# Kernel tuning notes

Measured on AMD Instinct MI355X. Metric: run time of the kernel, lower is better.

Reference implementation:

```python
import jax, jax.numpy as jnp
import numpy as np

B, N, C = 2, 2048, 1024
H = 16
D = C // H  # head_dim = 64

def setup_inputs() -> dict:
    key = jax.random.key(0)
    ks = jax.random.split(key, 5)
    s = 0.02
    return {
        "x": jax.random.normal(ks[0], (B, N, C), dtype=jnp.float32),
        "qkv_w": jax.random.normal(ks[1], (C, 3 * C), dtype=jnp.float32) * s,
        "qkv_b": jax.random.normal(ks[2], (3 * C,), dtype=jnp.float32) * s,
        "proj_w": jax.random.normal(ks[3], (C, C), dtype=jnp.float32) * s,
        "proj_b": jax.random.normal(ks[4], (C,), dtype=jnp.float32) * s,
    }

def reference(x, qkv_w, qkv_b, proj_w, proj_b):
    b, n, c = x.shape
    scale = (c // H) ** -0.5
    qkv = x @ qkv_w + qkv_b                      # (B, N, 3C)
    qkv = qkv.reshape(b, n, 3, H, D)
    q, k, v = jnp.moveaxis(qkv, 2, 0)            # each (B, N, H, D)
    # scores: (B, H, N, N)
    attn = jnp.einsum('bnhd,bmhd->bhnm', q, k) * scale
    attn = jax.nn.softmax(attn, axis=-1)
    out = jnp.einsum('bhnm,bmhd->bnhd', attn, v).reshape(b, n, c)
    out = out @ proj_w + proj_b
    return out
```

## Files before the change

kernel.cpp:

```cpp
#include <hip/hip_runtime.h>
#include <cstdint>
#include <cstddef>

typedef __bf16 bf16x8 __attribute__((ext_vector_type(8)));
typedef __bf16 bf16x2v __attribute__((ext_vector_type(2)));
typedef unsigned short u16;
typedef u16 u16x8v __attribute__((ext_vector_type(8)));
typedef float  f32x4  __attribute__((ext_vector_type(4)));
typedef unsigned int u32;

#define MFMA16(a, b, c) __builtin_amdgcn_mfma_f32_16x16x32_bf16((a), (b), (c), 0, 0, 0)
#define ASYNC16(g, l)                                                              \
  __builtin_amdgcn_global_load_lds(                                                \
      (const __attribute__((address_space(1))) unsigned int*)(g),                  \
      (__attribute__((address_space(3))) unsigned int*)(l), 16, 0, 0)

__device__ __forceinline__ u16 f2bf(float f) {
  unsigned u = __builtin_bit_cast(unsigned, f);
  u += 0x7fffu + ((u >> 16) & 1u);
  return (u16)(u >> 16);
}

__device__ __forceinline__ u32 cvt2(float a, float b) {
  bf16x2v t;
  t[0] = (__bf16)a;
  t[1] = (__bf16)b;
  return __builtin_bit_cast(u32, t);
}

#define SEQ 2048
#define CH  1024
#define NH  16
#define HD  64
#define QSCALE 0.18033688011112042f

__global__ void __launch_bounds__(256) prep_kernel(const float* __restrict__ x,
                                                   const float* __restrict__ qkv_w,
                                                   const float* __restrict__ proj_w,
                                                   u16* __restrict__ xb,
                                                   u16* __restrict__ wqkvt,
                                                   u16* __restrict__ wprojt) {
  __shared__ u16 t[64][68];
  int bx = blockIdx.x;
  int tx = threadIdx.x;
  if (bx < 4096) {
    int i = bx * 256 + tx;
    float4 v = ((const float4*)x)[i];
    ushort4 o;
    o.x = f2bf(v.x); o.y = f2bf(v.y); o.z = f2bf(v.z); o.w = f2bf(v.w);
    ((ushort4*)xb)[i] = o;
    return;
  }
  const float* in; u16* out; int R, C, c0, r0;
  if (bx < 4096 + 768) {
    int i = bx - 4096;
    in = qkv_w; out = wqkvt; R = 1024; C = 3072;
    c0 = (i % 48) * 64; r0 = (i / 48) * 64;
  } else {
    int i = bx - 4864;
    in = proj_w; out = wprojt; R = 1024; C = 1024;
    c0 = (i % 16) * 64; r0 = (i / 16) * 64;
  }
  int rr = tx >> 6, cc = tx & 63;
#pragma unroll
  for (int i = 0; i < 16; ++i) {
    int r = i * 4 + rr;
    t[r][cc] = f2bf(in[(size_t)(r0 + r) * C + c0 + cc]);
  }
  __syncthreads();
#pragma unroll
  for (int i = 0; i < 16; ++i) {
    int r = i * 4 + rr;
    out[(size_t)(c0 + r) * R + r0 + cc] = t[cc][r];
  }
}

template <int MT>
__global__ void __launch_bounds__(256) gemm_kernel(const u16* __restrict__ A,
                                                   const u16* __restrict__ Bt,
                                                   const float* __restrict__ bias,
                                                   u16* __restrict__ qk,
                                                   u16* __restrict__ vtout,
                                                   float* __restrict__ outf,
                                                   int K, int mode) {
  constexpr int R = MT * 32;
  __shared__ alignas(16) u16 smem[2 * R * 64 + 2 * 128 * 64];
  auto As = (u16(*)[R * 64])smem;
  auto Bs = (u16(*)[128 * 64])(smem + 2 * R * 64);
  int tid = threadIdx.x;
  int lane = tid & 63, wave = tid >> 6;
  int wm = wave >> 1, wn = wave & 1;
  int qr = lane & 15, quad = lane >> 4;
  size_t rowA = (size_t)blockIdx.y * R;
  size_t rowB = (size_t)blockIdx.x * 128;

  int klr = lane >> 3;
  int kcs = (lane & 7) ^ klr;

  f32x4 acc[MT][4];
#pragma unroll
  for (int mt = 0; mt < MT; ++mt)
#pragma unroll
    for (int nt = 0; nt < 4; ++nt) acc[mt][nt] = (f32x4){0.f, 0.f, 0.f, 0.f};

  auto stage = [&](int buf, int k0) {
#pragma unroll
    for (int i = 0; i < R / 32; ++i) {
      int ar = wave * (R / 4) + i * 8;
      ASYNC16(A + (rowA + ar + klr) * K + k0 + kcs * 8, &As[buf][ar * 64 + lane * 8]);
    }
#pragma unroll
    for (int i = 0; i < 4; ++i) {
      int br = wave * 32 + i * 8;
      ASYNC16(Bt + (rowB + br + klr) * K + k0 + kcs * 8, &Bs[buf][br * 64 + lane * 8]);
    }
  };

  stage(0, 0);
  int iters = K >> 6;
  for (int t = 0; t < iters; ++t) {
    int cur = t & 1;
    __syncthreads();
    if (t + 1 < iters) stage(cur ^ 1, (t + 1) * 64);
#pragma unroll
    for (int ks = 0; ks < 2; ++ks) {
      bf16x8 af[MT], bfr[4];
#pragma unroll
      for (int mt = 0; mt < MT; ++mt) {
        int row = wm * (MT * 16) + mt * 16 + qr;
        af[mt] = *(const bf16x8*)&As[cur][row * 64 + (((ks * 4 + quad) ^ (qr & 7)) << 3)];
      }
#pragma unroll
      for (int nt = 0; nt < 4; ++nt) {
        int row = wn * 64 + nt * 16 + qr;
        bfr[nt] = *(const bf16x8*)&Bs[cur][row * 64 + (((ks * 4 + quad) ^ (qr & 7)) << 3)];
      }
#pragma unroll
      for (int mt = 0; mt < MT; ++mt)
#pragma unroll
        for (int nt = 0; nt < 4; ++nt)
          acc[mt][nt] = MFMA16(af[mt], bfr[nt], acc[mt][nt]);
    }
    __syncthreads();
  }

  __syncthreads();

  if (mode == 1) {
    float* epf = (float*)smem;
#pragma unroll
    for (int nt = 0; nt < 4; ++nt) {
      int cl = wn * 64 + nt * 16 + qr;
      float bv = bias[rowB + cl];
#pragma unroll
      for (int mt = 0; mt < MT; ++mt) {
        int rl = wm * (MT * 16) + mt * 16 + quad * 4;
#pragma unroll
        for (int r = 0; r < 4; ++r)
          epf[(rl + r) * 132 + cl] = acc[mt][nt][r] + bv;
      }
    }
    __syncthreads();
    int rr = wave * 2 + (lane >> 5);
    int cc = (lane & 31) * 4;
#pragma unroll
    for (int p = 0; p < R / 8; ++p) {
      int row = p * 8 + rr;
      float4 v = *(const float4*)&epf[row * 132 + cc];
      *(float4*)&outf[(rowA + row) * 1024 + rowB + cc] = v;
    }
  } else if ((int)rowB < 2048) {
    float sc = ((int)rowB < 1024) ? QSCALE : 1.0f;
    u16* ep = smem;
#pragma unroll
    for (int nt = 0; nt < 4; ++nt) {
      int cl = wn * 64 + nt * 16 + qr;
      float bv = bias[rowB + cl];
#pragma unroll
      for (int mt = 0; mt < MT; ++mt) {
        int rl = wm * (MT * 16) + mt * 16 + quad * 4;
#pragma unroll
        for (int r = 0; r < 4; ++r)
          ep[(rl + r) * 136 + cl] = f2bf((acc[mt][nt][r] + bv) * sc);
      }
    }
    __syncthreads();
    int rr = wave * 4 + (lane >> 4);
    int cc = (lane & 15) * 8;
#pragma unroll
    for (int p = 0; p < R / 16; ++p) {
      int row = p * 16 + rr;
      u16x8v v = *(const u16x8v*)&ep[row * 136 + cc];
      *(u16x8v*)&qk[(rowA + row) * 2048 + rowB + cc] = v;
    }
  } else {
    u16* ep = smem;
#pragma unroll
    for (int nt = 0; nt < 4; ++nt) {
      int cl = wn * 64 + nt * 16 + qr;
      float bv = bias[rowB + cl];
#pragma unroll
      for (int mt = 0; mt < MT; ++mt) {
        int rl = wm * (MT * 16) + mt * 16 + quad * 4;
        ushort4 pv;
        pv.x = f2bf(acc[mt][nt][0] + bv);
        pv.y = f2bf(acc[mt][nt][1] + bv);
        pv.z = f2bf(acc[mt][nt][2] + bv);
        pv.w = f2bf(acc[mt][nt][3] + bv);
        *(ushort4*)&ep[cl * 136 + rl] = pv;
      }
    }
    __syncthreads();
    int batch = (int)(rowA >> 11);
    int n_base = (int)(rowA & 2047);
    int rr = wave * 4 + (lane >> 4);
    int cc = (lane & 15) * 8;
#pragma unroll
    for (int p = 0; p < 8; ++p) {
      int d = p * 16 + rr;
      int cglob = (int)rowB - 2048 + d;
      int bh_ = batch * 16 + (cglob >> 6);
      u16x8v v = *(const u16x8v*)&ep[d * 136 + cc];
      *(u16x8v*)&vtout[(size_t)bh_ * 131072 + (size_t)(cglob & 63) * 2048 + n_base + cc] = v;
    }
  }
}

__global__ void __launch_bounds__(256) attn_kernel(const u16* __restrict__ qkbuf,
                                                   const u16* __restrict__ vt,
                                                   u16* __restrict__ out) {
  __shared__ alignas(16) u16 kbuf[2][128 * 64];
  __shared__ alignas(16) u16 vbuf[2][64 * 128];
  __shared__ alignas(16) u16 pbuf[4][32 * 64];
  int bh = blockIdx.x;
  int b = bh >> 4, h = bh & 15;
  int m0 = blockIdx.y * 128;
  int tid = threadIdx.x;
  int lane = tid & 63, wave = tid >> 6;
  int qr = lane & 15, quad = lane >> 4;

  const u16* kbase = qkbuf + (size_t)(b * SEQ) * 2048 + 1024 + h * 64;
  const u16* vtbase = vt + (size_t)bh * 64 * SEQ;
  u16* pw = &pbuf[wave][0];

  int klr = lane >> 3;
  int kcs = (lane & 7) ^ klr;

  const u16* qbase = qkbuf + (size_t)(b * SEQ + m0 + wave * 32) * 2048 + h * 64;
  bf16x8 qf[2][2];
#pragma unroll
  for (int mt = 0; mt < 2; ++mt)
#pragma unroll
    for (int ks = 0; ks < 2; ++ks)
      qf[mt][ks] = *(const bf16x8*)&qbase[(size_t)(mt * 16 + qr) * 2048 + ks * 32 + quad * 8];

  const bf16x8 vone = __builtin_bit_cast(bf16x8, (u16x8v)((u16)0x3F80));

  f32x4 o[2][4], l5[2];
#pragma unroll
  for (int mt = 0; mt < 2; ++mt) {
    l5[mt] = (f32x4){0.f, 0.f, 0.f, 0.f};
#pragma unroll
    for (int dt = 0; dt < 4; ++dt) o[mt][dt] = (f32x4){0.f, 0.f, 0.f, 0.f};
  }

  auto stage = [&](int buf, int n0) {
#pragma unroll
    for (int i = 0; i < 4; ++i) {
      int kr = wave * 32 + i * 8 + klr;
      ASYNC16(kbase + (size_t)(n0 + kr) * 2048 + kcs * 8,
              &kbuf[buf][(wave * 32 + i * 8) * 64 + lane * 8]);
    }
#pragma unroll
    for (int i = 0; i < 4; ++i) {
      int vr = wave * 16 + i * 4 + (lane >> 4);
      int vcs = ((lane & 7) ^ (vr & 7)) | (lane & 8);
      ASYNC16(vtbase + (size_t)vr * 2048 + n0 + vcs * 8,
              &vbuf[buf][(wave * 16 + i * 4) * 128 + lane * 8]);
    }
  };

  stage(0, 0);

  for (int t = 0; t < 16; ++t) {
    int cur = t & 1;
    __syncthreads();

    if (t + 1 < 16) stage(cur ^ 1, (t + 1) * 128);

#pragma unroll
    for (int sp = 0; sp < 2; ++sp) {
      const u16* kb = &kbuf[cur][sp * 64 * 64];
      const u16* vb = &vbuf[cur][0];

      bf16x8 kf[4][2];
#pragma unroll
      for (int nt = 0; nt < 4; ++nt)
#pragma unroll
        for (int ks = 0; ks < 2; ++ks)
          kf[nt][ks] =
              *(const bf16x8*)&kb[(nt * 16 + qr) * 64 + (((ks * 4 + quad) ^ (qr & 7)) << 3)];

#pragma unroll
      for (int mt = 0; mt < 2; ++mt)
#pragma unroll
        for (int nt = 0; nt < 4; ++nt) {
          f32x4 z = (f32x4){0.f, 0.f, 0.f, 0.f};
          z = MFMA16(kf[nt][0], qf[mt][0], z);
          z = MFMA16(kf[nt][1], qf[mt][1], z);
          float p0 = __builtin_amdgcn_exp2f(z[0]);
          float p1 = __builtin_amdgcn_exp2f(z[1]);
          float p2 = __builtin_amdgcn_exp2f(z[2]);
          float p3 = __builtin_amdgcn_exp2f(z[3]);
          uint2 pk;
          pk.x = cvt2(p0, p1);
          pk.y = cvt2(p2, p3);
          int nb = nt * 16 + quad * 4;
          int addr = (mt * 16 + qr) * 64 + ((((nb >> 3) ^ (qr & 7)) << 3) | (nb & 7));
          *(uint2*)&pw[addr] = pk;
        }

      bf16x8 vf[4][2];
#pragma unroll
      for (int dt = 0; dt < 4; ++dt)
#pragma unroll
        for (int ks = 0; ks < 2; ++ks)
          vf[dt][ks] = *(const bf16x8*)&vb[(dt * 16 + qr) * 128 +
                                           ((sp * 8 + ((ks * 4 + quad) ^ (qr & 7))) << 3)];

      bf16x8 pf[2][2];
#pragma unroll
      for (int mt = 0; mt < 2; ++mt)
#pragma unroll
        for (int ks = 0; ks < 2; ++ks)
          pf[mt][ks] =
              *(const bf16x8*)&pw[(mt * 16 + qr) * 64 + (((ks * 4 + quad) ^ (qr & 7)) << 3)];

#pragma unroll
      for (int mt = 0; mt < 2; ++mt) {
#pragma unroll
        for (int dt = 0; dt < 4; ++dt) {
          o[mt][dt] = MFMA16(pf[mt][0], vf[dt][0], o[mt][dt]);
          o[mt][dt] = MFMA16(pf[mt][1], vf[dt][1], o[mt][dt]);
        }
        l5[mt] = MFMA16(pf[mt][0], vone, l5[mt]);
        l5[mt] = MFMA16(pf[mt][1], vone, l5[mt]);
      }
    }
  }

  u16* obase = out + (size_t)(b * SEQ + m0 + wave * 32) * CH + h * 64;
#pragma unroll
  for (int mt = 0; mt < 2; ++mt)
#pragma unroll
    for (int r = 0; r < 4; ++r) {
      float inv = 1.0f / l5[mt][r];
#pragma unroll
      for (int dt = 0; dt < 4; ++dt)
        obase[(size_t)(mt * 16 + quad * 4 + r) * CH + dt * 16 + qr] = f2bf(o[mt][dt][r] * inv);
    }
}

extern "C" void kernel_launch(void* const* d_in, const int* in_sizes, int n_in,
                              void* d_out, int out_size, void* d_ws, size_t ws_size,
                              hipStream_t stream) {
  const float* x      = (const float*)d_in[0];
  const float* qkv_w  = (const float*)d_in[1];
  const float* qkv_b  = (const float*)d_in[2];
  const float* proj_w = (const float*)d_in[3];
  const float* proj_b = (const float*)d_in[4];
  float* out = (float*)d_out;

  char* w = (char*)d_ws;
  u16* qkqk   = (u16*)w;
  u16* xb     = (u16*)(w + 16777216);
  u16* wprojt = (u16*)(w + 25165824);
  u16* wqkvt  = (u16*)(w + 27262976);
  u16* vt     = (u16*)(w + 33554432);
  u16* attn_bf = xb;

  prep_kernel<<<5120, 256, 0, stream>>>(x, qkv_w, proj_w, xb, wqkvt, wprojt);
  gemm_kernel<4><<<dim3(24, 32), 256, 0, stream>>>(xb, wqkvt, qkv_b, qkqk, vt, nullptr, 1024, 0);
  attn_kernel<<<dim3(32, 16), 256, 0, stream>>>(qkqk, vt, attn_bf);
  gemm_kernel<2><<<dim3(8, 64), 256, 0, stream>>>(attn_bf, wprojt, proj_b, nullptr, nullptr, out, 1024, 1);
}
```

Measured before the change: 179.9 us.

## Load K and V tiles directly from global memory instead of LDS staging

```diff
diff --git a/kernel.cpp b/kernel.cpp
--- a/kernel.cpp
+++ b/kernel.cpp
@@ -229,8 +229,6 @@
 __global__ void __launch_bounds__(256) attn_kernel(const u16* __restrict__ qkbuf,
                                                    const u16* __restrict__ vt,
                                                    u16* __restrict__ out) {
-  __shared__ alignas(16) u16 kbuf[2][128 * 64];
-  __shared__ alignas(16) u16 vbuf[2][64 * 128];
   __shared__ alignas(16) u16 pbuf[4][32 * 64];
   int bh = blockIdx.x;
   int b = bh >> 4, h = bh & 15;
@@ -243,9 +241,6 @@
   const u16* vtbase = vt + (size_t)bh * 64 * SEQ;
   u16* pw = &pbuf[wave][0];
 
-  int klr = lane >> 3;
-  int kcs = (lane & 7) ^ klr;
-
   const u16* qbase = qkbuf + (size_t)(b * SEQ + m0 + wave * 32) * 2048 + h * 64;
   bf16x8 qf[2][2];
 #pragma unroll
@@ -264,88 +259,61 @@
     for (int dt = 0; dt < 4; ++dt) o[mt][dt] = (f32x4){0.f, 0.f, 0.f, 0.f};
   }
 
-  auto stage = [&](int buf, int n0) {
-#pragma unroll
-    for (int i = 0; i < 4; ++i) {
-      int kr = wave * 32 + i * 8 + klr;
-      ASYNC16(kbase + (size_t)(n0 + kr) * 2048 + kcs * 8,
-              &kbuf[buf][(wave * 32 + i * 8) * 64 + lane * 8]);
-    }
-#pragma unroll
-    for (int i = 0; i < 4; ++i) {
-      int vr = wave * 16 + i * 4 + (lane >> 4);
-      int vcs = ((lane & 7) ^ (vr & 7)) | (lane & 8);
-      ASYNC16(vtbase + (size_t)vr * 2048 + n0 + vcs * 8,
-              &vbuf[buf][(wave * 16 + i * 4) * 128 + lane * 8]);
-    }
-  };
-
-  stage(0, 0);
-
-  for (int t = 0; t < 16; ++t) {
-    int cur = t & 1;
-    __syncthreads();
-
-    if (t + 1 < 16) stage(cur ^ 1, (t + 1) * 128);
-
-#pragma unroll
-    for (int sp = 0; sp < 2; ++sp) {
-      const u16* kb = &kbuf[cur][sp * 64 * 64];
-      const u16* vb = &vbuf[cur][0];
-
-      bf16x8 kf[4][2];
-#pragma unroll
-      for (int nt = 0; nt < 4; ++nt)
-#pragma unroll
-        for (int ks = 0; ks < 2; ++ks)
-          kf[nt][ks] =
-              *(const bf16x8*)&kb[(nt * 16 + qr) * 64 + (((ks * 4 + quad) ^ (qr & 7)) << 3)];
-
-#pragma unroll
-      for (int mt = 0; mt < 2; ++mt)
-#pragma unroll
-        for (int nt = 0; nt < 4; ++nt) {
-          f32x4 z = (f32x4){0.f, 0.f, 0.f, 0.f};
-          z = MFMA16(kf[nt][0], qf[mt][0], z);
-          z = MFMA16(kf[nt][1], qf[mt][1], z);
-          float p0 = __builtin_amdgcn_exp2f(z[0]);
-          float p1 = __builtin_amdgcn_exp2f(z[1]);
-          float p2 = __builtin_amdgcn_exp2f(z[2]);
-          float p3 = __builtin_amdgcn_exp2f(z[3]);
-          uint2 pk;
-          pk.x = cvt2(p0, p1);
-          pk.y = cvt2(p2, p3);
-          int nb = nt * 16 + quad * 4;
-          int addr = (mt * 16 + qr) * 64 + ((((nb >> 3) ^ (qr & 7)) << 3) | (nb & 7));
-          *(uint2*)&pw[addr] = pk;
-        }
-
-      bf16x8 vf[4][2];
-#pragma unroll
-      for (int dt = 0; dt < 4; ++dt)
-#pragma unroll
-        for (int ks = 0; ks < 2; ++ks)
-          vf[dt][ks] = *(const bf16x8*)&vb[(dt * 16 + qr) * 128 +
-                                           ((sp * 8 + ((ks * 4 + quad) ^ (qr & 7))) << 3)];
-
-      bf16x8 pf[2][2];
-#pragma unroll
-      for (int mt = 0; mt < 2; ++mt)
-#pragma unroll
-        for (int ks = 0; ks < 2; ++ks)
-          pf[mt][ks] =
-              *(const bf16x8*)&pw[(mt * 16 + qr) * 64 + (((ks * 4 + quad) ^ (qr & 7)) << 3)];
-
-#pragma unroll
-      for (int mt = 0; mt < 2; ++mt) {
-#pragma unroll
-        for (int dt = 0; dt < 4; ++dt) {
-          o[mt][dt] = MFMA16(pf[mt][0], vf[dt][0], o[mt][dt]);
-          o[mt][dt] = MFMA16(pf[mt][1], vf[dt][1], o[mt][dt]);
-        }
-        l5[mt] = MFMA16(pf[mt][0], vone, l5[mt]);
-        l5[mt] = MFMA16(pf[mt][1], vone, l5[mt]);
-      }
+  for (int t = 0; t < 32; ++t) {
+    const u16* kt = kbase + (size_t)(t * 64) * 2048;
+    const int n0 = t * 64;
+
+    bf16x8 kf[4][2];
+#pragma unroll
+    for (int nt = 0; nt < 4; ++nt)
+#pragma unroll
+      for (int ks = 0; ks < 2; ++ks)
+        kf[nt][ks] = *(const bf16x8*)&kt[(size_t)(nt * 16 + qr) * 2048 + ks * 32 + quad * 8];
+
+    bf16x8 vf[4][2];
+#pragma unroll
+    for (int dt = 0; dt < 4; ++dt)
+#pragma unroll
+      for (int ks = 0; ks < 2; ++ks)
+        vf[dt][ks] =
+            *(const bf16x8*)&vtbase[(size_t)(dt * 16 + qr) * 2048 + n0 + ks * 32 + quad * 8];
+
+#pragma unroll
+    for (int mt = 0; mt < 2; ++mt)
+#pragma unroll
+      for (int nt = 0; nt < 4; ++nt) {
+        f32x4 z = (f32x4){0.f, 0.f, 0.f, 0.f};
+        z = MFMA16(kf[nt][0], qf[mt][0], z);
+        z = MFMA16(kf[nt][1], qf[mt][1], z);
+        float p0 = __builtin_amdgcn_exp2f(z[0]);
+        float p1 = __builtin_amdgcn_exp2f(z[1]);
+        float p2 = __builtin_amdgcn_exp2f(z[2]);
+        float p3 = __builtin_amdgcn_exp2f(z[3]);
+        uint2 pk;
+        pk.x = cvt2(p0, p1);
+        pk.y = cvt2(p2, p3);
+        int nb = nt * 16 + quad * 4;
+        int addr = (mt * 16 + qr) * 64 + ((((nb >> 3) ^ (qr & 7)) << 3) | (nb & 7));
+        *(uint2*)&pw[addr] = pk;
+      }
+
+    bf16x8 pf[2][2];
+#pragma unroll
+    for (int mt = 0; mt < 2; ++mt)
+#pragma unroll
+      for (int ks = 0; ks < 2; ++ks)
+        pf[mt][ks] =
+            *(const bf16x8*)&pw[(mt * 16 + qr) * 64 + (((ks * 4 + quad) ^ (qr & 7)) << 3)];
+
+#pragma unroll
+    for (int mt = 0; mt < 2; ++mt) {
+#pragma unroll
+      for (int dt = 0; dt < 4; ++dt) {
+        o[mt][dt] = MFMA16(pf[mt][0], vf[dt][0], o[mt][dt]);
+        o[mt][dt] = MFMA16(pf[mt][1], vf[dt][1], o[mt][dt]);
+      }
+      l5[mt] = MFMA16(pf[mt][0], vone, l5[mt]);
+      l5[mt] = MFMA16(pf[mt][1], vone, l5[mt]);
     }
   }
 
```

Result: slower. 246.7 us (+37.1%).

## Add 256x256-tile 8-wave GEMM for QKV projection with double-buffered LDS pipeline

Applied to the files above, without the earlier changes.

```diff
diff --git a/kernel.cpp b/kernel.cpp
--- a/kernel.cpp
+++ b/kernel.cpp
@@ -226,6 +226,184 @@
   }
 }
 
+#define G256_LDSA(buf, ks)                                                         \
+  {                                                                                \
+    const u16* base_ = &smem[(buf) * 2 * 8192 + wm * 8192];                        \
+    _Pragma("unroll") for (int mt = 0; mt < 8; ++mt)                               \
+        afr[mt] = *(const bf16x8*)&base_[(mt * 16 + qr) * 64 +                     \
+                                         ((((ks) * 4 + quad) ^ (qr & 7)) << 3)];   \
+  }
+#define G256_LDSB(buf, ks, np)                                                     \
+  {                                                                                \
+    const u16* base_ = &smem[32768 + (buf) * 2 * 8192 + (wn >> 1) * 8192];         \
+    _Pragma("unroll") for (int u = 0; u < 2; ++u)                                  \
+        bfr[u] = *(const bf16x8*)&base_[((wn & 1) * 64 + ((np) * 2 + u) * 16 + qr) * 64 + \
+                                        ((((ks) * 4 + quad) ^ (qr & 7)) << 3)];    \
+  }
+#define G256_MMA(np)                                                               \
+  {                                                                                \
+    __builtin_amdgcn_s_setprio(1);                                                 \
+    _Pragma("unroll") for (int mt = 0; mt < 8; ++mt) {                             \
+      acc[mt][(np) * 2] = MFMA16(afr[mt], bfr[0], acc[mt][(np) * 2]);              \
+      acc[mt][(np) * 2 + 1] = MFMA16(afr[mt], bfr[1], acc[mt][(np) * 2 + 1]);      \
+    }                                                                              \
+    __builtin_amdgcn_s_setprio(0);                                                 \
+  }
+#define G256_STAGE_A(buf, t)                                                       \
+  _Pragma("unroll") for (int h = 0; h < 2; ++h)                                    \
+  _Pragma("unroll") for (int i = 0; i < 2; ++i) {                                  \
+    int rl = i * 64 + wave * 8;                                                    \
+    ASYNC16(A + (rowA + h * 128 + rl + klr) * 1024 + (t) * 64 + kcs * 8,           \
+            &smem[(buf) * 2 * 8192 + h * 8192 + rl * 64 + lane * 8]);              \
+  }
+#define G256_STAGE_B(buf, t)                                                       \
+  _Pragma("unroll") for (int h = 0; h < 2; ++h)                                    \
+  _Pragma("unroll") for (int i = 0; i < 2; ++i) {                                  \
+    int rl = i * 64 + wave * 8;                                                    \
+    ASYNC16(Bt + (rowB + h * 128 + rl + klr) * 1024 + (t) * 64 + kcs * 8,          \
+            &smem[32768 + (buf) * 2 * 8192 + h * 8192 + rl * 64 + lane * 8]);      \
+  }
+#define G256_BAR() __builtin_amdgcn_s_barrier()
+#define G256_VM0() asm volatile("s_waitcnt vmcnt(0)" ::: "memory")
+
+__global__ void __launch_bounds__(512) gemm256_kernel(const u16* __restrict__ A,
+                                                      const u16* __restrict__ Bt,
+                                                      const float* __restrict__ bias,
+                                                      u16* __restrict__ qk,
+                                                      u16* __restrict__ vtout) {
+  __shared__ alignas(16) u16 smem[65536];
+  int tid = threadIdx.x;
+  int lane = tid & 63, wave = tid >> 6;
+  int wm = wave >> 2, wn = wave & 3;
+  int qr = lane & 15, quad = lane >> 4;
+  int klr = lane >> 3;
+  int kcs = (lane & 7) ^ klr;
+
+  size_t rowA = (size_t)blockIdx.y * 256;
+  size_t rowB = (size_t)blockIdx.x * 256;
+
+  f32x4 acc[8][4];
+#pragma unroll
+  for (int mt = 0; mt < 8; ++mt)
+#pragma unroll
+    for (int nt = 0; nt < 4; ++nt) acc[mt][nt] = (f32x4){0.f, 0.f, 0.f, 0.f};
+
+  bf16x8 afr[8], bfr[2];
+
+  G256_STAGE_A(0, 0);
+  G256_STAGE_B(0, 0);
+  G256_VM0();
+
+  for (int j = 0; j < 8; ++j) {
+    G256_BAR();
+    G256_STAGE_A(1, 2 * j + 1);
+    G256_STAGE_B(1, 2 * j + 1);
+    G256_LDSA(0, 0);
+    G256_LDSB(0, 0, 0);
+    G256_MMA(0);
+    G256_BAR();
+    G256_LDSB(0, 0, 1);
+    G256_MMA(1);
+    G256_BAR();
+    G256_LDSA(0, 1);
+    G256_LDSB(0, 1, 0);
+    G256_MMA(0);
+    G256_BAR();
+    G256_LDSB(0, 1, 1);
+    G256_MMA(1);
+    G256_VM0();
+    G256_BAR();
+    if (j + 1 < 8) {
+      G256_STAGE_A(0, 2 * j + 2);
+      G256_STAGE_B(0, 2 * j + 2);
+    }
+    G256_LDSA(1, 0);
+    G256_LDSB(1, 0, 0);
+    G256_MMA(0);
+    G256_BAR();
+    G256_LDSB(1, 0, 1);
+    G256_MMA(1);
+    G256_BAR();
+    G256_LDSA(1, 1);
+    G256_LDSB(1, 1, 0);
+    G256_MMA(0);
+    G256_BAR();
+    G256_LDSB(1, 1, 1);
+    G256_MMA(1);
+    G256_VM0();
+  }
+  __syncthreads();
+
+  int bx = blockIdx.x;
+  float bv[4];
+#pragma unroll
+  for (int nt = 0; nt < 4; ++nt) bv[nt] = bias[rowB + wn * 64 + nt * 16 + qr];
+
+  u16* ep = smem;
+  if (bx < 8) {
+    float sc = (bx < 4) ? QSCALE : 1.0f;
+#pragma unroll
+    for (int cm = 0; cm < 2; ++cm) {
+      if (wm == cm) {
+#pragma unroll
+        for (int mt = 0; mt < 8; ++mt)
+#pragma unroll
+          for (int nt = 0; nt < 4; ++nt) {
+            int rl = mt * 16 + quad * 4;
+            int cl = wn * 64 + nt * 16 + qr;
+#pragma unroll
+            for (int r = 0; r < 4; ++r)
+              ep[(rl + r) * 264 + cl] = f2bf((acc[mt][nt][r] + bv[nt]) * sc);
+          }
+      }
+      __syncthreads();
+      int row = tid >> 5;
+      int c0 = (tid & 31) * 8;
+#pragma unroll
+      for (int p = 0; p < 8; ++p) {
+        int rr = p * 16 + row;
+        u16x8v v = *(const u16x8v*)&ep[rr * 264 + c0];
+        *(u16x8v*)&qk[(rowA + cm * 128 + rr) * 2048 + rowB + c0] = v;
+      }
+      __syncthreads();
+    }
+  } else {
+    int batch = (int)(rowA >> 11);
+    int n_base = (int)(rowA & 2047);
+    int dbase = (int)rowB - 2048;
+#pragma unroll
+    for (int cd = 0; cd < 2; ++cd) {
+      if ((wn >> 1) == cd) {
+#pragma unroll
+        for (int mt = 0; mt < 8; ++mt)
+#pragma unroll
+          for (int nt = 0; nt < 4; ++nt) {
+            int dl = (wn & 1) * 64 + nt * 16 + qr;
+            int nl = wm * 128 + mt * 16 + quad * 4;
+            ushort4 pv;
+            pv.x = f2bf(acc[mt][nt][0] + bv[nt]);
+            pv.y = f2bf(acc[mt][nt][1] + bv[nt]);
+            pv.z = f2bf(acc[mt][nt][2] + bv[nt]);
+            pv.w = f2bf(acc[mt][nt][3] + bv[nt]);
+            *(ushort4*)&ep[dl * 264 + nl] = pv;
+          }
+      }
+      __syncthreads();
+      int dl = tid >> 5;
+      int n0 = (tid & 31) * 8;
+#pragma unroll
+      for (int p = 0; p < 8; ++p) {
+        int dd = p * 16 + dl;
+        int dglob = dbase + cd * 128 + dd;
+        int bh_ = batch * 16 + (dglob >> 6);
+        u16x8v v = *(const u16x8v*)&ep[dd * 264 + n0];
+        *(u16x8v*)&vtout[(size_t)bh_ * 131072 + (size_t)(dglob & 63) * 2048 + n_base + n0] = v;
+      }
+      __syncthreads();
+    }
+  }
+}
+
 __global__ void __launch_bounds__(256) attn_kernel(const u16* __restrict__ qkbuf,
                                                    const u16* __restrict__ vt,
                                                    u16* __restrict__ out) {
@@ -380,7 +558,7 @@
   u16* attn_bf = xb;
 
   prep_kernel<<<5120, 256, 0, stream>>>(x, qkv_w, proj_w, xb, wqkvt, wprojt);
-  gemm_kernel<4><<<dim3(24, 32), 256, 0, stream>>>(xb, wqkvt, qkv_b, qkqk, vt, nullptr, 1024, 0);
+  gemm256_kernel<<<dim3(12, 16), 512, 0, stream>>>(xb, wqkvt, qkv_b, qkqk, vt);
   attn_kernel<<<dim3(32, 16), 256, 0, stream>>>(qkqk, vt, attn_bf);
   gemm_kernel<2><<<dim3(8, 64), 256, 0, stream>>>(attn_bf, wprojt, proj_b, nullptr, nullptr, out, 1024, 1);
 }
```

Result: no change. 182.8 us (+1.6%).

## Split attention work across eight waves with sixteen query rows each

Applied to the files above, without the earlier changes.

```diff
diff --git a/kernel.cpp b/kernel.cpp
--- a/kernel.cpp
+++ b/kernel.cpp
@@ -226,12 +226,12 @@
   }
 }
 
-__global__ void __launch_bounds__(256) attn_kernel(const u16* __restrict__ qkbuf,
-                                                   const u16* __restrict__ vt,
-                                                   u16* __restrict__ out) {
+__global__ void __launch_bounds__(512, 4) attn_kernel(const u16* __restrict__ qkbuf,
+                                                      const u16* __restrict__ vt,
+                                                      u16* __restrict__ out) {
   __shared__ alignas(16) u16 kbuf[2][128 * 64];
   __shared__ alignas(16) u16 vbuf[2][64 * 128];
-  __shared__ alignas(16) u16 pbuf[4][32 * 64];
+  __shared__ alignas(16) u16 pbuf[8][16 * 64];
   int bh = blockIdx.x;
   int b = bh >> 4, h = bh & 15;
   int m0 = blockIdx.y * 128;
@@ -246,37 +246,32 @@
   int klr = lane >> 3;
   int kcs = (lane & 7) ^ klr;
 
-  const u16* qbase = qkbuf + (size_t)(b * SEQ + m0 + wave * 32) * 2048 + h * 64;
-  bf16x8 qf[2][2];
-#pragma unroll
-  for (int mt = 0; mt < 2; ++mt)
-#pragma unroll
-    for (int ks = 0; ks < 2; ++ks)
-      qf[mt][ks] = *(const bf16x8*)&qbase[(size_t)(mt * 16 + qr) * 2048 + ks * 32 + quad * 8];
+  const u16* qbase = qkbuf + (size_t)(b * SEQ + m0 + wave * 16) * 2048 + h * 64;
+  bf16x8 qf[2];
+#pragma unroll
+  for (int ks = 0; ks < 2; ++ks)
+    qf[ks] = *(const bf16x8*)&qbase[(size_t)qr * 2048 + ks * 32 + quad * 8];
 
   const bf16x8 vone = __builtin_bit_cast(bf16x8, (u16x8v)((u16)0x3F80));
 
-  f32x4 o[2][4], l5[2];
-#pragma unroll
-  for (int mt = 0; mt < 2; ++mt) {
-    l5[mt] = (f32x4){0.f, 0.f, 0.f, 0.f};
-#pragma unroll
-    for (int dt = 0; dt < 4; ++dt) o[mt][dt] = (f32x4){0.f, 0.f, 0.f, 0.f};
-  }
+  f32x4 o[4], l5;
+  l5 = (f32x4){0.f, 0.f, 0.f, 0.f};
+#pragma unroll
+  for (int dt = 0; dt < 4; ++dt) o[dt] = (f32x4){0.f, 0.f, 0.f, 0.f};
 
   auto stage = [&](int buf, int n0) {
 #pragma unroll
-    for (int i = 0; i < 4; ++i) {
-      int kr = wave * 32 + i * 8 + klr;
+    for (int i = 0; i < 2; ++i) {
+      int kr = wave * 16 + i * 8 + klr;
       ASYNC16(kbase + (size_t)(n0 + kr) * 2048 + kcs * 8,
-              &kbuf[buf][(wave * 32 + i * 8) * 64 + lane * 8]);
-    }
-#pragma unroll
-    for (int i = 0; i < 4; ++i) {
-      int vr = wave * 16 + i * 4 + (lane >> 4);
+              &kbuf[buf][(wave * 16 + i * 8) * 64 + lane * 8]);
+    }
+#pragma unroll
+    for (int i = 0; i < 2; ++i) {
+      int vr = wave * 8 + i * 4 + (lane >> 4);
       int vcs = ((lane & 7) ^ (vr & 7)) | (lane & 8);
       ASYNC16(vtbase + (size_t)vr * 2048 + n0 + vcs * 8,
-              &vbuf[buf][(wave * 16 + i * 4) * 128 + lane * 8]);
+              &vbuf[buf][(wave * 8 + i * 4) * 128 + lane * 8]);
     }
   };
 
@@ -302,23 +297,21 @@
               *(const bf16x8*)&kb[(nt * 16 + qr) * 64 + (((ks * 4 + quad) ^ (qr & 7)) << 3)];
 
 #pragma unroll
-      for (int mt = 0; mt < 2; ++mt)
-#pragma unroll
-        for (int nt = 0; nt < 4; ++nt) {
-          f32x4 z = (f32x4){0.f, 0.f, 0.f, 0.f};
-          z = MFMA16(kf[nt][0], qf[mt][0], z);
-          z = MFMA16(kf[nt][1], qf[mt][1], z);
-          float p0 = __builtin_amdgcn_exp2f(z[0]);
-          float p1 = __builtin_amdgcn_exp2f(z[1]);
-          float p2 = __builtin_amdgcn_exp2f(z[2]);
-          float p3 = __builtin_amdgcn_exp2f(z[3]);
-          uint2 pk;
-          pk.x = cvt2(p0, p1);
-          pk.y = cvt2(p2, p3);
-          int nb = nt * 16 + quad * 4;
-          int addr = (mt * 16 + qr) * 64 + ((((nb >> 3) ^ (qr & 7)) << 3) | (nb & 7));
-          *(uint2*)&pw[addr] = pk;
-        }
+      for (int nt = 0; nt < 4; ++nt) {
+        f32x4 z = (f32x4){0.f, 0.f, 0.f, 0.f};
+        z = MFMA16(kf[nt][0], qf[0], z);
+        z = MFMA16(kf[nt][1], qf[1], z);
+        float p0 = __builtin_amdgcn_exp2f(z[0]);
+        float p1 = __builtin_amdgcn_exp2f(z[1]);
+        float p2 = __builtin_amdgcn_exp2f(z[2]);
+        float p3 = __builtin_amdgcn_exp2f(z[3]);
+        uint2 pk;
+        pk.x = cvt2(p0, p1);
+        pk.y = cvt2(p2, p3);
+        int nb = nt * 16 + quad * 4;
+        int addr = qr * 64 + ((((nb >> 3) ^ (qr & 7)) << 3) | (nb & 7));
+        *(uint2*)&pw[addr] = pk;
+      }
 
       bf16x8 vf[4][2];
 #pragma unroll
@@ -328,37 +321,29 @@
           vf[dt][ks] = *(const bf16x8*)&vb[(dt * 16 + qr) * 128 +
                                            ((sp * 8 + ((ks * 4 + quad) ^ (qr & 7))) << 3)];
 
-      bf16x8 pf[2][2];
-#pragma unroll
-      for (int mt = 0; mt < 2; ++mt)
-#pragma unroll
-        for (int ks = 0; ks < 2; ++ks)
-          pf[mt][ks] =
-              *(const bf16x8*)&pw[(mt * 16 + qr) * 64 + (((ks * 4 + quad) ^ (qr & 7)) << 3)];
-
-#pragma unroll
-      for (int mt = 0; mt < 2; ++mt) {
-#pragma unroll
-        for (int dt = 0; dt < 4; ++dt) {
-          o[mt][dt] = MFMA16(pf[mt][0], vf[dt][0], o[mt][dt]);
-          o[mt][dt] = MFMA16(pf[mt][1], vf[dt][1], o[mt][dt]);
-        }
-        l5[mt] = MFMA16(pf[mt][0], vone, l5[mt]);
-        l5[mt] = MFMA16(pf[mt][1], vone, l5[mt]);
-      }
-    }
-  }
-
-  u16* obase = out + (size_t)(b * SEQ + m0 + wave * 32) * CH + h * 64;
-#pragma unroll
-  for (int mt = 0; mt < 2; ++mt)
-#pragma unroll
-    for (int r = 0; r < 4; ++r) {
-      float inv = 1.0f / l5[mt][r];
-#pragma unroll
-      for (int dt = 0; dt < 4; ++dt)
-        obase[(size_t)(mt * 16 + quad * 4 + r) * CH + dt * 16 + qr] = f2bf(o[mt][dt][r] * inv);
-    }
+      bf16x8 pf[2];
+#pragma unroll
+      for (int ks = 0; ks < 2; ++ks)
+        pf[ks] = *(const bf16x8*)&pw[qr * 64 + (((ks * 4 + quad) ^ (qr & 7)) << 3)];
+
+#pragma unroll
+      for (int dt = 0; dt < 4; ++dt) {
+        o[dt] = MFMA16(pf[0], vf[dt][0], o[dt]);
+        o[dt] = MFMA16(pf[1], vf[dt][1], o[dt]);
+      }
+      l5 = MFMA16(pf[0], vone, l5);
+      l5 = MFMA16(pf[1], vone, l5);
+    }
+  }
+
+  u16* obase = out + (size_t)(b * SEQ + m0 + wave * 16) * CH + h * 64;
+#pragma unroll
+  for (int r = 0; r < 4; ++r) {
+    float inv = 1.0f / l5[r];
+#pragma unroll
+    for (int dt = 0; dt < 4; ++dt)
+      obase[(size_t)(quad * 4 + r) * CH + dt * 16 + qr] = f2bf(o[dt][r] * inv);
+  }
 }
 
 extern "C" void kernel_launch(void* const* d_in, const int* in_sizes, int n_in,
@@ -381,6 +366,6 @@
 
   prep_kernel<<<5120, 256, 0, stream>>>(x, qkv_w, proj_w, xb, wqkvt, wprojt);
   gemm_kernel<4><<<dim3(24, 32), 256, 0, stream>>>(xb, wqkvt, qkv_b, qkqk, vt, nullptr, 1024, 0);
-  attn_kernel<<<dim3(32, 16), 256, 0, stream>>>(qkqk, vt, attn_bf);
+  attn_kernel<<<dim3(32, 16), 512, 0, stream>>>(qkqk, vt, attn_bf);
   gemm_kernel<2><<<dim3(8, 64), 256, 0, stream>>>(attn_bf, wprojt, proj_b, nullptr, nullptr, out, 1024, 1);
 }
```

New measurement: 177.7 us. Within noise of the previous version (-1.2%).
